# Kernel tuning notes

Hardware: AMD Instinct MI355X
Metric: run time of the kernel (lower is better)

Reference implementation:

```python
import jax, jax.numpy as jnp
import numpy as np

CODE_DIMS = [32, 32, 16]   # prod = 16384 out features
FEAT_DIM = 1024
EPS = 1e-6


def setup_inputs() -> dict:
    key = jax.random.key(0)
    kx, kw = jax.random.split(key)
    x = jax.random.normal(kx, (4, 2048, FEAT_DIM), dtype=jnp.float32)
    # per-chunk trunc-normal init like _init_weights: std = sqrt(2/(feat_dim+code_dim)), clipped at +-3 std
    parts = []
    for i, cd in enumerate(CODE_DIMS):
        std = float(np.sqrt(2.0 / (FEAT_DIM + cd)))
        parts.append(std * jax.random.truncated_normal(
            jax.random.fold_in(kw, i), -3.0, 3.0, (cd, FEAT_DIM), dtype=jnp.float32))
    weight = jnp.concatenate(parts, axis=0)  # (sum(code_dims)=80, feat_dim)
    return {"x": x, "weight": weight}


def _rms_norm(y):
    var = jnp.mean(y * y, axis=-1, keepdims=True) + EPS
    return y * jax.lax.rsqrt(var)


def reference(x, weight):
    # split weight rows into the low-rank factors
    a, b, c = jnpp_split = jnp.split(weight, np.cumsum(CODE_DIMS)[:-1].tolist(), axis=0)
    # outer product over code dims, shared feature axis z -> dynamic weight (prod(code_dims), feat_dim)
    W = jnp.einsum('az,bz,cz->abcz', a, b, c).reshape(-1, weight.shape[-1])
    y = jnp.einsum('bsi,oi->bso', x, W)  # dense projection
    return _rms_norm(y)
```

## Files before the change

### kernel.cpp

```cpp
#include <hip/hip_runtime.h>
#include <hip/hip_bf16.h>

typedef unsigned short u16;
typedef __attribute__((ext_vector_type(8))) short bf16x8;
typedef __attribute__((ext_vector_type(4))) float f32x4;
typedef __attribute__((ext_vector_type(8))) unsigned short ushort8;

#define FEAT 1024
#define NOUT 16384
#define EPS 1e-6f
#define NT 32

#define GLOBAL_AS __attribute__((address_space(1)))
#define LDS_AS __attribute__((address_space(3)))

__device__ __forceinline__ void load16_to_lds(const u16* g, u16* l) {
    __builtin_amdgcn_global_load_lds((const GLOBAL_AS void*)g, (LDS_AS void*)l, 16, 0, 0);
}

__device__ __forceinline__ u16 f32_to_bf16_bits(float f) {
    __hip_bfloat16 h = __float2bfloat16(f);
    return *reinterpret_cast<u16*>(&h);
}

__device__ __forceinline__ float bf16_bits_to_f32(u16 b) {
    unsigned u = ((unsigned)b) << 16;
    float f;
    __builtin_memcpy(&f, &u, 4);
    return f;
}

__global__ void wbuild_kernel(const float* __restrict__ w, u16* __restrict__ Wb) {
    const int t  = blockIdx.x * 256 + threadIdx.x;
    const int p  = t >> 7;
    const int k0 = (t & 127) << 3;
    const int o  = (p & ~63) | ((p & 15) << 2) | ((p >> 4) & 3);
    const int ai = o >> 9;
    const int bi = (o >> 4) & 31;
    const int ci = o & 15;
    const float* A = w + ai * FEAT + k0;
    const float* B = w + (32 + bi) * FEAT + k0;
    const float* C = w + (64 + ci) * FEAT + k0;
    ushort8 r;
#pragma unroll
    for (int j = 0; j < 8; ++j) r[j] = f32_to_bf16_bits(A[j] * B[j] * C[j]);
    *reinterpret_cast<ushort8*>(Wb + (size_t)t * 8) = r;
}

__global__ void xcast_kernel(const float* __restrict__ x, u16* __restrict__ Xb) {
    const int t = blockIdx.x * 256 + threadIdx.x;
    const float4* xv = reinterpret_cast<const float4*>(x) + (size_t)t * 2;
    const float4 f0 = xv[0];
    const float4 f1 = xv[1];
    float vals[8] = {f0.x, f0.y, f0.z, f0.w, f1.x, f1.y, f1.z, f1.w};
    ushort8 r;
#pragma unroll
    for (int j = 0; j < 8; ++j) r[j] = f32_to_bf16_bits(vals[j]);
    *reinterpret_cast<ushort8*>(Xb + (size_t)t * 8) = r;
}


#define LA(buf) (lds + (buf) * 12288)
#define LB(buf) (lds + (buf) * 12288 + 8192)

#define STAGE(tt, buf) do {                                                   \
    const int ko = (tt) * 32;                                                 \
    load16_to_lds(gA0 + ko, LA(buf) + w * 512);                               \
    load16_to_lds(gA1 + ko, LA(buf) + 4096 + w * 512);                        \
    load16_to_lds(gB0 + ko, LB(buf) + w * 512);                               \
} while (0)

#define RD_A(dst, mi, buf) dst = *reinterpret_cast<const bf16x8*>(            \
    LA(buf) + (wm * 64 + (mi) * 16 + fr) * 32 + ((kg ^ ((fr >> 1) & 3)) << 3))
#define RD_B(dst, nj, buf) dst = *reinterpret_cast<const bf16x8*>(            \
    LB(buf) + (wn * 64 + (nj) * 16 + fr) * 32 + ((kg ^ ((fr >> 1) & 3)) << 3))

#define BAR() do {                                                            \
    __builtin_amdgcn_sched_barrier(0);                                        \
    __builtin_amdgcn_s_barrier();                                             \
    __builtin_amdgcn_sched_barrier(0);                                        \
} while (0)

#define TILE(t, buf) do {                                                     \
    bf16x8 a0, a1, a2, a3, b0, b1, b2, b3;                                    \
    RD_A(a0, 0, buf); RD_A(a1, 1, buf); RD_A(a2, 2, buf); RD_A(a3, 3, buf);   \
    RD_B(b0, 0, buf); RD_B(b1, 1, buf); RD_B(b2, 2, buf); RD_B(b3, 3, buf);   \
    __builtin_amdgcn_s_setprio(1);                                            \
    acc[0][0] = __builtin_amdgcn_mfma_f32_16x16x32_bf16(a0, b0, acc[0][0], 0, 0, 0); \
    acc[0][1] = __builtin_amdgcn_mfma_f32_16x16x32_bf16(a0, b1, acc[0][1], 0, 0, 0); \
    acc[0][2] = __builtin_amdgcn_mfma_f32_16x16x32_bf16(a0, b2, acc[0][2], 0, 0, 0); \
    acc[0][3] = __builtin_amdgcn_mfma_f32_16x16x32_bf16(a0, b3, acc[0][3], 0, 0, 0); \
    acc[1][0] = __builtin_amdgcn_mfma_f32_16x16x32_bf16(a1, b0, acc[1][0], 0, 0, 0); \
    acc[1][1] = __builtin_amdgcn_mfma_f32_16x16x32_bf16(a1, b1, acc[1][1], 0, 0, 0); \
    acc[1][2] = __builtin_amdgcn_mfma_f32_16x16x32_bf16(a1, b2, acc[1][2], 0, 0, 0); \
    acc[1][3] = __builtin_amdgcn_mfma_f32_16x16x32_bf16(a1, b3, acc[1][3], 0, 0, 0); \
    acc[2][0] = __builtin_amdgcn_mfma_f32_16x16x32_bf16(a2, b0, acc[2][0], 0, 0, 0); \
    acc[2][1] = __builtin_amdgcn_mfma_f32_16x16x32_bf16(a2, b1, acc[2][1], 0, 0, 0); \
    acc[2][2] = __builtin_amdgcn_mfma_f32_16x16x32_bf16(a2, b2, acc[2][2], 0, 0, 0); \
    acc[2][3] = __builtin_amdgcn_mfma_f32_16x16x32_bf16(a2, b3, acc[2][3], 0, 0, 0); \
    acc[3][0] = __builtin_amdgcn_mfma_f32_16x16x32_bf16(a3, b0, acc[3][0], 0, 0, 0); \
    acc[3][1] = __builtin_amdgcn_mfma_f32_16x16x32_bf16(a3, b1, acc[3][1], 0, 0, 0); \
    acc[3][2] = __builtin_amdgcn_mfma_f32_16x16x32_bf16(a3, b2, acc[3][2], 0, 0, 0); \
    acc[3][3] = __builtin_amdgcn_mfma_f32_16x16x32_bf16(a3, b3, acc[3][3], 0, 0, 0); \
    __builtin_amdgcn_s_setprio(0);                                            \
    if ((t) < NT - 1) {                                                       \
        BAR();                                                                \
        if ((t) < NT - 2) {                                                   \
            STAGE((t) + 2, buf);                                              \
            asm volatile("s_waitcnt vmcnt(3)" ::: "memory");                  \
        } else {                                                              \
            asm volatile("s_waitcnt vmcnt(0)" ::: "memory");                  \
        }                                                                     \
        BAR();                                                                \
    }                                                                         \
} while (0)

__global__ __launch_bounds__(512, 4) void gemm_kernel(const u16* __restrict__ Xb,
                                                      const u16* __restrict__ Wb,
                                                      u16* __restrict__ Y) {
    __shared__ u16 lds[24576];

    const int tid  = threadIdx.x;
    const int lane = tid & 63;
    const int w    = tid >> 6;
    const int wm   = w >> 1;
    const int wn   = w & 1;
    const int fr   = lane & 15;
    const int kg   = lane >> 4;

    const int bid = blockIdx.x;
    const int xcd = bid & 7;
    const int o   = bid >> 3;
    const int cb  = xcd * 16 + (o >> 7) * 4 + (o & 3);
    const int rb  = (o >> 2) & 31;
    const int brow = rb * 256;
    const int bcol = cb * 128;

    const int srow = tid >> 2;
    const int kc   = (tid & 3) ^ ((srow >> 1) & 3);
    const u16* gA0 = Xb + (size_t)(brow + srow) * FEAT + kc * 8;
    const u16* gA1 = gA0 + 128 * FEAT;
    const u16* gB0 = Wb + (size_t)(bcol + srow) * FEAT + kc * 8;

    f32x4 acc[4][4] = {};

    STAGE(0, 0);
    STAGE(1, 1);
    asm volatile("s_waitcnt vmcnt(3)" ::: "memory");
    BAR();

#pragma unroll 2
    for (int tt = 0; tt < NT; ++tt) {
        TILE(tt, (tt & 1));
    }

    const int colbase = bcol + wn * 64 + fr * 4;
#pragma unroll
    for (int mi = 0; mi < 4; ++mi) {
#pragma unroll
        for (int r = 0; r < 4; ++r) {
            const int row = brow + wm * 64 + mi * 16 + kg * 4 + r;
            const unsigned lo = (unsigned)f32_to_bf16_bits(acc[mi][0][r]) |
                                ((unsigned)f32_to_bf16_bits(acc[mi][1][r]) << 16);
            const unsigned hi = (unsigned)f32_to_bf16_bits(acc[mi][2][r]) |
                                ((unsigned)f32_to_bf16_bits(acc[mi][3][r]) << 16);
            uint2 pk; pk.x = lo; pk.y = hi;
            *reinterpret_cast<uint2*>(Y + (size_t)row * 32768 + colbase) = pk;
        }
    }
}

__global__ __launch_bounds__(1024) void scale_kernel(const u16* __restrict__ Y,
                                                     float* __restrict__ out) {
    const int row = blockIdx.x;
    const int tid = threadIdx.x;
    const ushort8* yr = reinterpret_cast<const ushort8*>(Y + (size_t)row * 32768);
    const ushort8 v0 = yr[2 * tid];
    const ushort8 v1 = yr[2 * tid + 1];

    float f[16];
#pragma unroll
    for (int j = 0; j < 8; ++j) {
        f[j]     = bf16_bits_to_f32(v0[j]);
        f[8 + j] = bf16_bits_to_f32(v1[j]);
    }
    float ss = 0.f;
#pragma unroll
    for (int j = 0; j < 16; ++j) ss += f[j] * f[j];

#pragma unroll
    for (int off = 1; off < 64; off <<= 1) ss += __shfl_xor(ss, off, 64);
    __shared__ float wss[16];
    if ((tid & 63) == 0) wss[tid >> 6] = ss;
    __syncthreads();
    float tot = 0.f;
#pragma unroll
    for (int i = 0; i < 16; ++i) tot += wss[i];
    const float sc = rsqrtf(tot * (1.0f / (float)NOUT) + EPS);

    float4* orow = reinterpret_cast<float4*>(out + (size_t)row * NOUT) + tid * 4;
#pragma unroll
    for (int q = 0; q < 4; ++q) {
        float4 ov;
        ov.x = f[q * 4 + 0] * sc;
        ov.y = f[q * 4 + 1] * sc;
        ov.z = f[q * 4 + 2] * sc;
        ov.w = f[q * 4 + 3] * sc;
        orow[q] = ov;
    }
}

extern "C" void kernel_launch(void* const* d_in, const int* in_sizes, int n_in,
                              void* d_out, int out_size, void* d_ws, size_t ws_size,
                              hipStream_t stream) {
    const float* x = (const float*)d_in[0];
    const float* w = (const float*)d_in[1];
    float* out = (float*)d_out;

    const int M = in_sizes[0] / FEAT;

    u16* Wb = (u16*)d_ws;
    u16* Xb = (u16*)((char*)d_ws + (size_t)NOUT * FEAT * 2);

    u16* Y = (u16*)d_out;

    wbuild_kernel<<<(NOUT * (FEAT / 8)) / 256, 256, 0, stream>>>(w, Wb);
    xcast_kernel<<<(M * FEAT / 8) / 256, 256, 0, stream>>>(x, Xb);

    const int nblk = (M / 256) * (NOUT / 128);
    gemm_kernel<<<nblk, 512, 0, stream>>>(Xb, Wb, Y);

    scale_kernel<<<M, 1024, 0, stream>>>(Y, out);
}
```

Baseline: 466.9 us.

## Restructure GEMM to 128x256 tiles with K=64 triple-buffered LDS pipeline

The GEMM block tile changes from 256x128 to 128x256, the K step doubles to 64 with an 8-way XOR swizzle, and LDS goes from double to triple buffering. This halves the number of barriers per K. Within each step, loads are interleaved between the two K-halves, and even and odd waves process the halves in staggered order to spread LDS traffic. The weight-build and x-cast kernels are merged into one launch, removing a launch. The cost is more LDS per block, which lowers occupancy to 2 blocks per CU, and the M-derived grid sizes are now hardcoded.

```diff
diff --git a/kernel.cpp b/kernel.cpp
--- a/kernel.cpp
+++ b/kernel.cpp
@@ -9,7 +9,7 @@
 #define FEAT 1024
 #define NOUT 16384
 #define EPS 1e-6f
-#define NT 32
+#define NW 16
 
 #define GLOBAL_AS __attribute__((address_space(1)))
 #define LDS_AS __attribute__((address_space(3)))
@@ -30,50 +30,58 @@
     return f;
 }
 
-__global__ void wbuild_kernel(const float* __restrict__ w, u16* __restrict__ Wb) {
-    const int t  = blockIdx.x * 256 + threadIdx.x;
-    const int p  = t >> 7;
-    const int k0 = (t & 127) << 3;
-    const int o  = (p & ~63) | ((p & 15) << 2) | ((p >> 4) & 3);
-    const int ai = o >> 9;
-    const int bi = (o >> 4) & 31;
-    const int ci = o & 15;
-    const float* A = w + ai * FEAT + k0;
-    const float* B = w + (32 + bi) * FEAT + k0;
-    const float* C = w + (64 + ci) * FEAT + k0;
-    ushort8 r;
-#pragma unroll
-    for (int j = 0; j < 8; ++j) r[j] = f32_to_bf16_bits(A[j] * B[j] * C[j]);
-    *reinterpret_cast<ushort8*>(Wb + (size_t)t * 8) = r;
-}
-
-__global__ void xcast_kernel(const float* __restrict__ x, u16* __restrict__ Xb) {
-    const int t = blockIdx.x * 256 + threadIdx.x;
-    const float4* xv = reinterpret_cast<const float4*>(x) + (size_t)t * 2;
-    const float4 f0 = xv[0];
-    const float4 f1 = xv[1];
-    float vals[8] = {f0.x, f0.y, f0.z, f0.w, f1.x, f1.y, f1.z, f1.w};
-    ushort8 r;
-#pragma unroll
-    for (int j = 0; j < 8; ++j) r[j] = f32_to_bf16_bits(vals[j]);
-    *reinterpret_cast<ushort8*>(Xb + (size_t)t * 8) = r;
-}
-
-
-#define LA(buf) (lds + (buf) * 12288)
-#define LB(buf) (lds + (buf) * 12288 + 8192)
-
-#define STAGE(tt, buf) do {                                                   \
-    const int ko = (tt) * 32;                                                 \
-    load16_to_lds(gA0 + ko, LA(buf) + w * 512);                               \
-    load16_to_lds(gA1 + ko, LA(buf) + 4096 + w * 512);                        \
-    load16_to_lds(gB0 + ko, LB(buf) + w * 512);                               \
-} while (0)
-
-#define RD_A(dst, mi, buf) dst = *reinterpret_cast<const bf16x8*>(            \
-    LA(buf) + (wm * 64 + (mi) * 16 + fr) * 32 + ((kg ^ ((fr >> 1) & 3)) << 3))
-#define RD_B(dst, nj, buf) dst = *reinterpret_cast<const bf16x8*>(            \
-    LB(buf) + (wn * 64 + (nj) * 16 + fr) * 32 + ((kg ^ ((fr >> 1) & 3)) << 3))
+__global__ void prep_kernel(const float* __restrict__ w, u16* __restrict__ Wb,
+                            const float* __restrict__ x, u16* __restrict__ Xb) {
+    const int bid = blockIdx.x;
+    if (bid < 8192) {
+        const int t  = bid * 256 + threadIdx.x;
+        const int p  = t >> 7;
+        const int k0 = (t & 127) << 3;
+        const int o  = (p & ~63) | ((p & 15) << 2) | ((p >> 4) & 3);
+        const int ai = o >> 9;
+        const int bi = (o >> 4) & 31;
+        const int ci = o & 15;
+        const float* A = w + ai * FEAT + k0;
+        const float* B = w + (32 + bi) * FEAT + k0;
+        const float* C = w + (64 + ci) * FEAT + k0;
+        ushort8 r;
+#pragma unroll
+        for (int j = 0; j < 8; ++j) r[j] = f32_to_bf16_bits(A[j] * B[j] * C[j]);
+        *reinterpret_cast<ushort8*>(Wb + (size_t)t * 8) = r;
+    } else {
+        const int t = (bid - 8192) * 256 + threadIdx.x;
+        const float4* xv = reinterpret_cast<const float4*>(x) + (size_t)t * 2;
+        const float4 f0 = xv[0];
+        const float4 f1 = xv[1];
+        float vals[8] = {f0.x, f0.y, f0.z, f0.w, f1.x, f1.y, f1.z, f1.w};
+        ushort8 r;
+#pragma unroll
+        for (int j = 0; j < 8; ++j) r[j] = f32_to_bf16_bits(vals[j]);
+        *reinterpret_cast<ushort8*>(Xb + (size_t)t * 8) = r;
+    }
+}
+
+
+#define WSZ 24576
+
+#define STAGE_A(tt, nb) do {                                                  \
+    const u16* g = gAs + (size_t)(tt) * 64;                                   \
+    load16_to_lds(g,             (nb) + wv * 512);                            \
+    load16_to_lds(g + 64 * FEAT, (nb) + 4096 + wv * 512);                     \
+} while (0)
+
+#define STAGE_B(tt, nb) do {                                                  \
+    const u16* g = gBs + (size_t)(tt) * 64;                                   \
+    load16_to_lds(g,               (nb) + 8192  + wv * 512);                  \
+    load16_to_lds(g + 64  * FEAT,  (nb) + 12288 + wv * 512);                  \
+    load16_to_lds(g + 128 * FEAT,  (nb) + 16384 + wv * 512);                  \
+    load16_to_lds(g + 192 * FEAT,  (nb) + 20480 + wv * 512);                  \
+} while (0)
+
+#define RD_A(dst, mi, kh, wb) dst = *reinterpret_cast<const bf16x8*>(         \
+    (wb) + (wm * 64 + (mi) * 16 + fr) * 64 + (((((kh) << 2) | kg)) ^ (fr & 7)) * 8)
+#define RD_B(dst, nj, kh, wb) dst = *reinterpret_cast<const bf16x8*>(         \
+    (wb) + 8192 + (wn * 64 + (nj) * 16 + fr) * 64 + (((((kh) << 2) | kg)) ^ (fr & 7)) * 8)
 
 #define BAR() do {                                                            \
     __builtin_amdgcn_sched_barrier(0);                                        \
@@ -81,10 +89,12 @@
     __builtin_amdgcn_sched_barrier(0);                                        \
 } while (0)
 
-#define TILE(t, buf) do {                                                     \
+#define HALFC(kh, wb) do {                                                    \
     bf16x8 a0, a1, a2, a3, b0, b1, b2, b3;                                    \
-    RD_A(a0, 0, buf); RD_A(a1, 1, buf); RD_A(a2, 2, buf); RD_A(a3, 3, buf);   \
-    RD_B(b0, 0, buf); RD_B(b1, 1, buf); RD_B(b2, 2, buf); RD_B(b3, 3, buf);   \
+    RD_A(a0, 0, kh, wb); RD_A(a1, 1, kh, wb);                                 \
+    RD_A(a2, 2, kh, wb); RD_A(a3, 3, kh, wb);                                 \
+    RD_B(b0, 0, kh, wb); RD_B(b1, 1, kh, wb);                                 \
+    RD_B(b2, 2, kh, wb); RD_B(b3, 3, kh, wb);                                 \
     __builtin_amdgcn_s_setprio(1);                                            \
     acc[0][0] = __builtin_amdgcn_mfma_f32_16x16x32_bf16(a0, b0, acc[0][0], 0, 0, 0); \
     acc[0][1] = __builtin_amdgcn_mfma_f32_16x16x32_bf16(a0, b1, acc[0][1], 0, 0, 0); \
@@ -103,55 +113,62 @@
     acc[3][2] = __builtin_amdgcn_mfma_f32_16x16x32_bf16(a3, b2, acc[3][2], 0, 0, 0); \
     acc[3][3] = __builtin_amdgcn_mfma_f32_16x16x32_bf16(a3, b3, acc[3][3], 0, 0, 0); \
     __builtin_amdgcn_s_setprio(0);                                            \
-    if ((t) < NT - 1) {                                                       \
-        BAR();                                                                \
-        if ((t) < NT - 2) {                                                   \
-            STAGE((t) + 2, buf);                                              \
-            asm volatile("s_waitcnt vmcnt(3)" ::: "memory");                  \
-        } else {                                                              \
-            asm volatile("s_waitcnt vmcnt(0)" ::: "memory");                  \
-        }                                                                     \
-        BAR();                                                                \
-    }                                                                         \
-} while (0)
-
-__global__ __launch_bounds__(512, 4) void gemm_kernel(const u16* __restrict__ Xb,
+} while (0)
+
+__global__ __launch_bounds__(512, 2) void gemm_kernel(const u16* __restrict__ Xb,
                                                       const u16* __restrict__ Wb,
                                                       u16* __restrict__ Y) {
-    __shared__ u16 lds[24576];
+    __shared__ u16 lds[3 * WSZ];
 
     const int tid  = threadIdx.x;
     const int lane = tid & 63;
-    const int w    = tid >> 6;
-    const int wm   = w >> 1;
-    const int wn   = w & 1;
+    const int wv   = tid >> 6;
+    const int wm   = wv >> 2;
+    const int wn   = wv & 3;
     const int fr   = lane & 15;
     const int kg   = lane >> 4;
+    const int stag = (wv ^ (wv >> 2)) & 1;
 
     const int bid = blockIdx.x;
     const int xcd = bid & 7;
     const int o   = bid >> 3;
-    const int cb  = xcd * 16 + (o >> 7) * 4 + (o & 3);
-    const int rb  = (o >> 2) & 31;
-    const int brow = rb * 256;
-    const int bcol = cb * 128;
-
-    const int srow = tid >> 2;
-    const int kc   = (tid & 3) ^ ((srow >> 1) & 3);
-    const u16* gA0 = Xb + (size_t)(brow + srow) * FEAT + kc * 8;
-    const u16* gA1 = gA0 + 128 * FEAT;
-    const u16* gB0 = Wb + (size_t)(bcol + srow) * FEAT + kc * 8;
+    const int cb  = xcd * 8 + (o >> 8) * 4 + (o & 3);
+    const int rb  = (o >> 2) & 63;
+    const int brow = rb * 128;
+    const int bcol = cb * 256;
+
+    const int srow = tid >> 3;
+    const int swz  = (lane & 7) ^ (lane >> 3);
+    const u16* gAs = Xb + (size_t)(brow + srow) * FEAT + swz * 8;
+    const u16* gBs = Wb + (size_t)(bcol + srow) * FEAT + swz * 8;
 
     f32x4 acc[4][4] = {};
 
-    STAGE(0, 0);
-    STAGE(1, 1);
-    asm volatile("s_waitcnt vmcnt(3)" ::: "memory");
+    STAGE_A(0, lds);
+    STAGE_B(0, lds);
+    STAGE_A(1, lds + WSZ);
+    STAGE_B(1, lds + WSZ);
+    asm volatile("s_waitcnt vmcnt(6)" ::: "memory");
     BAR();
 
-#pragma unroll 2
-    for (int tt = 0; tt < NT; ++tt) {
-        TILE(tt, (tt & 1));
+    int cur = 0;
+    for (int t = 0; t < NW; ++t) {
+        u16* wb = lds + cur * WSZ;
+        const int nxti = (cur + 2 >= 3) ? (cur - 1) : (cur + 2);
+        u16* nb = lds + nxti * WSZ;
+        const bool st = (t < NW - 2);
+        if (st) STAGE_A(t + 2, nb);
+        if (stag) { HALFC(1, wb); } else { HALFC(0, wb); }
+        if (st) STAGE_B(t + 2, nb);
+        if (stag) { HALFC(0, wb); } else { HALFC(1, wb); }
+        if (t < NW - 2) {
+            asm volatile("s_waitcnt vmcnt(6)" ::: "memory");
+            BAR();
+        } else if (t == NW - 2) {
+            asm volatile("s_waitcnt vmcnt(0)" ::: "memory");
+            BAR();
+        }
+        cur = (cur + 1 == 3) ? 0 : (cur + 1);
     }
 
     const int colbase = bcol + wn * 64 + fr * 4;
@@ -217,18 +234,15 @@
     const float* w = (const float*)d_in[1];
     float* out = (float*)d_out;
 
-    const int M = in_sizes[0] / FEAT;
-
     u16* Wb = (u16*)d_ws;
     u16* Xb = (u16*)((char*)d_ws + (size_t)NOUT * FEAT * 2);
 
     u16* Y = (u16*)d_out;
 
-    wbuild_kernel<<<(NOUT * (FEAT / 8)) / 256, 256, 0, stream>>>(w, Wb);
-    xcast_kernel<<<(M * FEAT / 8) / 256, 256, 0, stream>>>(x, Xb);
-
-    const int nblk = (M / 256) * (NOUT / 128);
+    prep_kernel<<<12288, 256, 0, stream>>>(w, Wb, x, Xb);
+
+    const int nblk = 4096;
     gemm_kernel<<<nblk, 512, 0, stream>>>(Xb, Wb, Y);
 
-    scale_kernel<<<M, 1024, 0, stream>>>(Y, out);
-}
+    scale_kernel<<<8192, 1024, 0, stream>>>(Y, out);
+}
```

Result: no change. 469.9 us (+0.6%).
